# Kernel optimization log

Hardware: AMD Instinct MI355X
Metric: run time of the kernel (lower is better)

## Reference

```python
import jax, jax.numpy as jnp
import numpy as np
from jax import lax

DIM = 512
D_STATE = 16
D_CONV = 4
EXPAND = 2
E = EXPAND * DIM  # expanded_dim


def setup_inputs() -> dict:
    key = jax.random.key(0)
    ks = jax.random.split(key, 8)
    B_, L = 4, 2048
    x = jax.random.normal(ks[0], (B_, L, DIM), dtype=jnp.float32)
    # parameters (xavier-ish scaled random; exact init values don't matter for math)
    W_in = jax.random.normal(ks[1], (2 * E, DIM), dtype=jnp.float32) * (1.0 / np.sqrt(DIM))
    W_conv = jax.random.normal(ks[2], (E, 1, D_CONV), dtype=jnp.float32) * 0.3
    A = jax.random.normal(ks[3], (E, D_STATE), dtype=jnp.float32) * 0.5
    Bp = jax.random.normal(ks[4], (E, D_STATE), dtype=jnp.float32) * (1.0 / np.sqrt(D_STATE))
    Cp = jax.random.normal(ks[5], (E, D_STATE), dtype=jnp.float32) * (1.0 / np.sqrt(D_STATE))
    Dp = jnp.zeros((E,), dtype=jnp.float32)
    W_out = jax.random.normal(ks[6], (DIM, E), dtype=jnp.float32) * (1.0 / np.sqrt(E))
    return {"x": x, "W_in": W_in, "W_conv": W_conv, "A": A, "Bp": Bp, "Cp": Cp, "Dp": Dp, "W_out": W_out}


def reference(x, W_in, W_conv, A, Bp, Cp, Dp, W_out):
    residual = x
    b, l, _ = x.shape
    xp = jnp.einsum('bld,ed->ble', x, W_in)        # [b,l,2E]
    xs, gate = jnp.split(xp, 2, axis=-1)
    xs = xs * jax.nn.sigmoid(gate)                 # [b,l,E]
    # causal depthwise conv1d: torch pads both sides by K-1 then slices [:, :, :l]
    xc = lax.conv_general_dilated(
        xs.transpose(0, 2, 1), W_conv,
        window_strides=(1,), padding=[(D_CONV - 1, 0)],
        feature_group_count=E,
        dimension_numbers=('NCH', 'OIH', 'NCH'))     # [b,E,l]
    u = jax.nn.silu(xc.transpose(0, 2, 1))          # [b,l,E]
    Aneg = -jnp.exp(A)                              # [E,N]
    delta = jax.nn.sigmoid(jnp.einsum('bld,dn->bln', u, Bp))  # [b,l,N]
    A_bar = jnp.exp(jnp.einsum('dn,bln->bldn', Aneg, delta))  # [b,l,E,N]
    Bx = jnp.einsum('bln,dn->bldn', delta, Bp) * u[..., None]  # B_bar * x_t

    def step(h, inp):
        A_t, Bx_t = inp
        h = A_t * h + Bx_t                          # [b,E,N]
        y_t = jnp.einsum('bdn,dn->bd', h, Cp)
        return h, y_t

    h0 = jnp.zeros((b, E, D_STATE), dtype=x.dtype)
    _, ys = lax.scan(step, h0, (A_bar.transpose(1, 0, 2, 3), Bx.transpose(1, 0, 2, 3)))
    y = ys.transpose(1, 0, 2)                       # [b,l,E]
    y = y + Dp * u
    out = jnp.einsum('ble,de->bld', y, W_out)
    return out + residual
```

## Files before the change

### kernel.cpp

```cpp
#include <hip/hip_runtime.h>

#define DIM   512
#define EE    1024
#define NS    16
#define BB    4
#define LL    2048
#define MM    (BB*LL)
#define NC    64
#define CL    32

typedef __bf16 bf16x8 __attribute__((ext_vector_type(8)));
typedef __bf16 bf16x4 __attribute__((ext_vector_type(4)));
typedef float  f32x4  __attribute__((ext_vector_type(4)));

static __device__ __forceinline__ float sigmoidf_(float x) {
    return 1.0f / (1.0f + __expf(-x));
}

#define GLOAD(gp, lp) __builtin_amdgcn_global_load_lds( \
    (const __attribute__((address_space(1))) unsigned int*)(const void*)(gp), \
    (__attribute__((address_space(3))) unsigned int*)(void*)(lp), 16, 0, 0)

__global__ __launch_bounds__(256) void k_tobf(
    const float* __restrict__ x, const float* __restrict__ Win,
    const float* __restrict__ Wout, const float* __restrict__ Bp,
    __bf16* __restrict__ xbf, __bf16* __restrict__ winbf,
    __bf16* __restrict__ woutbf, __bf16* __restrict__ bpT)
{
    int g = blockIdx.x * 256 + threadIdx.x;
    const int nx4 = MM * DIM / 4;
    const int nw4 = 2 * EE * DIM / 4;
    const int no4 = DIM * EE / 4;
    if (g < nx4) {
        f32x4 v = ((const f32x4*)x)[g];
        bf16x4 o; for (int j = 0; j < 4; ++j) o[j] = (__bf16)v[j];
        ((bf16x4*)xbf)[g] = o;
    } else if (g < nx4 + nw4) {
        int i = g - nx4;
        f32x4 v = ((const f32x4*)Win)[i];
        bf16x4 o; for (int j = 0; j < 4; ++j) o[j] = (__bf16)v[j];
        ((bf16x4*)winbf)[i] = o;
    } else if (g < nx4 + nw4 + no4) {
        int i = g - nx4 - nw4;
        f32x4 v = ((const f32x4*)Wout)[i];
        bf16x4 o; for (int j = 0; j < 4; ++j) o[j] = (__bf16)v[j];
        ((bf16x4*)woutbf)[i] = o;
    } else {
        int i = g - nx4 - nw4 - no4;
        int e = i >> 4, n = i & 15;
        bpT[n * EE + e] = (__bf16)Bp[i];
    }
}

__global__ __launch_bounds__(256, 4) void k_gemm1(
    const __bf16* __restrict__ Abf,
    const __bf16* __restrict__ Wbf,
    __bf16* __restrict__ xs)
{
    __shared__ __bf16 sA[128 * 64];
    __shared__ __bf16 sB0[64 * 64];
    __shared__ __bf16 sB1[64 * 64];

    int bid = blockIdx.x;
    int swz = (bid & 7) * 128 + (bid >> 3);
    int bm = swz >> 4;
    int bn = swz & 15;

    int t = threadIdx.x;
    int lane = t & 63;
    int w = t >> 6;
    int wm = (w >> 1) * 64;
    int wn = (w & 1) * 32;
    int r15 = lane & 15;
    int kq = lane >> 4;

    const __bf16* Agb  = Abf + (bm * 128) * DIM;
    const __bf16* B0gb = Wbf + (bn * 64) * DIM;
    const __bf16* B1gb = Wbf + (1024 + bn * 64) * DIM;

    f32x4 accx[4][2] = {};
    f32x4 accg[4][2] = {};

    for (int kt = 0; kt < 8; ++kt) {
        #pragma unroll
        for (int i_ = 0; i_ < 4; ++i_) {
            int c_ = i_ * 256 + t;
            int row_ = c_ >> 3;
            int ss_ = (c_ & 7) ^ (row_ & 7);
            GLOAD(Agb + kt * 64 + row_ * DIM + ss_ * 8, sA + (i_ * 256 + w * 64) * 8);
        }
        #pragma unroll
        for (int i_ = 0; i_ < 2; ++i_) {
            int c_ = i_ * 256 + t;
            int row_ = c_ >> 3;
            int ss_ = (c_ & 7) ^ (row_ & 7);
            GLOAD(B0gb + kt * 64 + row_ * DIM + ss_ * 8, sB0 + (i_ * 256 + w * 64) * 8);
            GLOAD(B1gb + kt * 64 + row_ * DIM + ss_ * 8, sB1 + (i_ * 256 + w * 64) * 8);
        }
        __syncthreads();
        #pragma unroll
        for (int ks = 0; ks < 2; ++ks) {
            int kcs = ks * 4 + kq;
            bf16x8 a[4], b0[2], b1[2];
            #pragma unroll
            for (int m = 0; m < 4; ++m) {
                int r = wm + m * 16 + r15;
                a[m] = *(const bf16x8*)&sA[r * 64 + (kcs ^ (r & 7)) * 8];
            }
            #pragma unroll
            for (int n = 0; n < 2; ++n) {
                int r = wn + n * 16 + r15;
                b0[n] = *(const bf16x8*)&sB0[r * 64 + (kcs ^ (r & 7)) * 8];
                b1[n] = *(const bf16x8*)&sB1[r * 64 + (kcs ^ (r & 7)) * 8];
            }
            #pragma unroll
            for (int m = 0; m < 4; ++m)
                #pragma unroll
                for (int n = 0; n < 2; ++n) {
                    accx[m][n] = __builtin_amdgcn_mfma_f32_16x16x32_bf16(a[m], b0[n], accx[m][n], 0, 0, 0);
                    accg[m][n] = __builtin_amdgcn_mfma_f32_16x16x32_bf16(a[m], b1[n], accg[m][n], 0, 0, 0);
                }
        }
        __syncthreads();
    }

    #pragma unroll
    for (int m = 0; m < 4; ++m)
        #pragma unroll
        for (int n = 0; n < 2; ++n)
            #pragma unroll
            for (int r = 0; r < 4; ++r) {
                int row = bm * 128 + wm + m * 16 + (lane >> 4) * 4 + r;
                int col = bn * 64 + wn + n * 16 + r15;
                float xv = accx[m][n][r];
                float gv = accg[m][n][r];
                xs[row * EE + col] = (__bf16)(xv * sigmoidf_(gv));
            }
}

__global__ __launch_bounds__(256) void k_convdelta(
    const __bf16* __restrict__ xs, const float* __restrict__ Wc,
    const __bf16* __restrict__ bpT,
    __bf16* __restrict__ u, float* __restrict__ delta)
{
    __shared__ __bf16 uS[8][1032];
    __shared__ float red[4][256];
    int bid = blockIdx.x;
    int r0b = bid * 8;
    int t = threadIdx.x;
    int cg = t & 127, rh = t >> 7;
    int e8 = cg << 3;
    int rr0 = r0b + rh * 4;
    int l0 = rr0 & (LL - 1);

    f32x4 wj[8];
    #pragma unroll
    for (int j = 0; j < 8; ++j) wj[j] = *(const f32x4*)&Wc[(e8 + j) * 4];
    bf16x8 z = {};
    bf16x8 win[7];
    #pragma unroll
    for (int i = 0; i < 7; ++i) {
        win[i] = (l0 + i >= 3) ? *(const bf16x8*)&xs[(rr0 + i - 3) * EE + e8] : z;
    }
    #pragma unroll
    for (int i = 0; i < 4; ++i) {
        bf16x8 out;
        #pragma unroll
        for (int j = 0; j < 8; ++j) {
            float a = (float)win[i][j] * wj[j][0] + (float)win[i + 1][j] * wj[j][1]
                    + (float)win[i + 2][j] * wj[j][2] + (float)win[i + 3][j] * wj[j][3];
            out[j] = (__bf16)(a * sigmoidf_(a));
        }
        *(bf16x8*)&u[(rr0 + i) * EE + e8] = out;
        *(bf16x8*)&uS[rh * 4 + i][e8] = out;
    }
    __syncthreads();

    int lane = t & 63, w = t >> 6;
    int ar = lane & 15, kc = (lane >> 4) << 3;
    f32x4 acc = {};
    #pragma unroll
    for (int k0 = 0; k0 < 256; k0 += 32) {
        int k = w * 256 + k0 + kc;
        bf16x8 a = *(const bf16x8*)&uS[ar & 7][k];
        bf16x8 b = *(const bf16x8*)&bpT[ar * EE + k];
        acc = __builtin_amdgcn_mfma_f32_16x16x32_bf16(a, b, acc, 0, 0, 0);
    }
    *(f32x4*)&red[w][lane * 4] = acc;
    __syncthreads();
    if (t < 32) {
        #pragma unroll
        for (int r = 0; r < 4; ++r) {
            float s = red[0][t * 4 + r] + red[1][t * 4 + r]
                    + red[2][t * 4 + r] + red[3][t * 4 + r];
            int row = (t >> 4) * 4 + r;
            int col = t & 15;
            delta[(r0b + row) * NS + col] = sigmoidf_(s);
        }
    }
}

__global__ __launch_bounds__(64) void k_dsum(
    const float* __restrict__ delta, float* __restrict__ Dsum)
{
    int g = blockIdx.x * 64 + threadIdx.x;
    int n = g & 15, c = (g >> 4) & (NC - 1), b = g >> 10;
    int base = (b * LL + c * CL) * NS + n;
    float s = 0.f;
    #pragma unroll
    for (int l = 0; l < CL; ++l) s += delta[base + l * NS];
    Dsum[(b * NC + c) * NS + n] = s;
}

__global__ __launch_bounds__(256) void k_scan1(
    const __bf16* __restrict__ u, const float* __restrict__ delta,
    const float* __restrict__ A, const float* __restrict__ Bp,
    const float* __restrict__ Cp, const float* __restrict__ Dp,
    float* __restrict__ hbuf, __bf16* __restrict__ yloc)
{
    int bid = blockIdx.x;
    int et = bid & 3;
    int c  = (bid >> 2) & (NC - 1);
    int b  = bid >> 8;
    int t  = threadIdx.x;
    int e  = et * 256 + t;
    __shared__ float dls[CL * NS];
    int sbase = (b * LL + c * CL) * NS;
    for (int i = t; i < CL * NS; i += 256) dls[i] = delta[sbase + i];
    __syncthreads();

    float Ae[NS], Bpr[NS], Cr[NS];
    #pragma unroll
    for (int q = 0; q < 4; ++q) {
        f32x4 av = *(const f32x4*)&A[e * NS + q * 4];
        f32x4 bv = *(const f32x4*)&Bp[e * NS + q * 4];
        f32x4 cv = *(const f32x4*)&Cp[e * NS + q * 4];
        #pragma unroll
        for (int j = 0; j < 4; ++j) {
            Ae[q * 4 + j]  = -__expf(av[j]) * 1.44269504f;
            Bpr[q * 4 + j] = bv[j];
            Cr[q * 4 + j]  = cv[j];
        }
    }
    float Dv = Dp[e];
    float h[NS] = {};
    const __bf16* up = &u[(b * LL + c * CL) * EE + e];
    __bf16* yp = &yloc[(b * LL + c * CL) * EE + e];
    for (int l = 0; l < CL; ++l) {
        float uv = (float)up[l * EE];
        float yv = Dv * uv;
        const f32x4* dr = (const f32x4*)&dls[l * NS];
        f32x4 dv[4] = {dr[0], dr[1], dr[2], dr[3]};
        #pragma unroll
        for (int j = 0; j < NS; ++j) {
            float d  = dv[j >> 2][j & 3];
            float ab = __builtin_amdgcn_exp2f(Ae[j] * d);
            h[j] = ab * h[j] + (d * Bpr[j]) * uv;
            yv += h[j] * Cr[j];
        }
        yp[l * EE] = (__bf16)yv;
    }
    int base = ((b * NC + c) * EE + e) * NS;
    #pragma unroll
    for (int q = 0; q < 4; ++q) {
        f32x4 hv = {h[q * 4 + 0], h[q * 4 + 1], h[q * 4 + 2], h[q * 4 + 3]};
        *(f32x4*)&hbuf[base + q * 4] = hv;
    }
}

__global__ __launch_bounds__(256) void k_fix(
    const float* __restrict__ A, const float* __restrict__ Dsum,
    float* __restrict__ hbuf)
{
    int g = blockIdx.x * 256 + threadIdx.x;
    int b = g >> 14;
    int r = g & 16383;
    int n = r & 15;
    float Ae = -__expf(A[r]) * 1.44269504f;
    float h = 0.f;
    for (int c = 0; c < NC; ++c) {
        int idx = (b * NC + c) * (EE * NS) + r;
        float hl = hbuf[idx];
        float P  = __builtin_amdgcn_exp2f(Ae * Dsum[(b * NC + c) * NS + n]);
        hbuf[idx] = h;
        h = P * h + hl;
    }
}

__global__ __launch_bounds__(256) void k_scan2(
    const float* __restrict__ delta, const float* __restrict__ A,
    const float* __restrict__ Cp, const float* __restrict__ hin,
    __bf16* __restrict__ y)
{
    int bid = blockIdx.x;
    int et = bid & 3;
    int c  = (bid >> 2) & (NC - 1);
    int b  = bid >> 8;
    if (c == 0) return;
    int t  = threadIdx.x;
    int e  = et * 256 + t;
    __shared__ float dls[CL * NS];
    int sbase = (b * LL + c * CL) * NS;
    for (int i = t; i < CL * NS; i += 256) dls[i] = delta[sbase + i];
    __syncthreads();

    int base = ((b * NC + c) * EE + e) * NS;
    float Ae[NS], g_[NS];
    #pragma unroll
    for (int q = 0; q < 4; ++q) {
        f32x4 av = *(const f32x4*)&A[e * NS + q * 4];
        f32x4 cv = *(const f32x4*)&Cp[e * NS + q * 4];
        f32x4 hv = *(const f32x4*)&hin[base + q * 4];
        #pragma unroll
        for (int j = 0; j < 4; ++j) {
            Ae[q * 4 + j] = -__expf(av[j]) * 1.44269504f;
            g_[q * 4 + j] = cv[j] * hv[j];
        }
    }
    float D[NS] = {};
    __bf16* yp = &y[(b * LL + c * CL) * EE + e];
    for (int l = 0; l < CL; ++l) {
        const f32x4* dr = (const f32x4*)&dls[l * NS];
        f32x4 dv[4] = {dr[0], dr[1], dr[2], dr[3]};
        float corr = 0.f;
        #pragma unroll
        for (int j = 0; j < NS; ++j) {
            D[j] += dv[j >> 2][j & 3];
            corr += g_[j] * __builtin_amdgcn_exp2f(Ae[j] * D[j]);
        }
        float yv = (float)yp[l * EE] + corr;
        yp[l * EE] = (__bf16)yv;
    }
}

__global__ __launch_bounds__(256, 2) void k_gemm2(
    const __bf16* __restrict__ Ybf,
    const __bf16* __restrict__ Wobf,
    const float* __restrict__ xres,
    float* __restrict__ out)
{
    __shared__ __bf16 sA[128 * 64];
    __shared__ __bf16 sB[64 * 64];

    int bid = blockIdx.x;
    int swz = (bid & 7) * 64 + (bid >> 3);
    int bm = swz >> 3;
    int bn = swz & 7;

    int t = threadIdx.x;
    int lane = t & 63;
    int w = t >> 6;
    int wm = (w >> 1) * 64;
    int wn = (w & 1) * 32;
    int r15 = lane & 15;
    int kq = lane >> 4;

    const __bf16* Agb = Ybf + (bm * 128) * EE;
    const __bf16* Bgb = Wobf + (bn * 64) * EE;

    f32x4 acc[4][2] = {};

    for (int kt = 0; kt < 16; ++kt) {
        #pragma unroll
        for (int i_ = 0; i_ < 4; ++i_) {
            int c_ = i_ * 256 + t;
            int row_ = c_ >> 3;
            int ss_ = (c_ & 7) ^ (row_ & 7);
            GLOAD(Agb + kt * 64 + row_ * EE + ss_ * 8, sA + (i_ * 256 + w * 64) * 8);
        }
        #pragma unroll
        for (int i_ = 0; i_ < 2; ++i_) {
            int c_ = i_ * 256 + t;
            int row_ = c_ >> 3;
            int ss_ = (c_ & 7) ^ (row_ & 7);
            GLOAD(Bgb + kt * 64 + row_ * EE + ss_ * 8, sB + (i_ * 256 + w * 64) * 8);
        }
        __syncthreads();
        #pragma unroll
        for (int ks = 0; ks < 2; ++ks) {
            int kcs = ks * 4 + kq;
            bf16x8 a[4], b[2];
            #pragma unroll
            for (int m = 0; m < 4; ++m) {
                int r = wm + m * 16 + r15;
                a[m] = *(const bf16x8*)&sA[r * 64 + (kcs ^ (r & 7)) * 8];
            }
            #pragma unroll
            for (int n = 0; n < 2; ++n) {
                int r = wn + n * 16 + r15;
                b[n] = *(const bf16x8*)&sB[r * 64 + (kcs ^ (r & 7)) * 8];
            }
            #pragma unroll
            for (int m = 0; m < 4; ++m)
                #pragma unroll
                for (int n = 0; n < 2; ++n)
                    acc[m][n] = __builtin_amdgcn_mfma_f32_16x16x32_bf16(a[m], b[n], acc[m][n], 0, 0, 0);
        }
        __syncthreads();
    }

    #pragma unroll
    for (int m = 0; m < 4; ++m)
        #pragma unroll
        for (int n = 0; n < 2; ++n)
            #pragma unroll
            for (int r = 0; r < 4; ++r) {
                int row = bm * 128 + wm + m * 16 + (lane >> 4) * 4 + r;
                int col = bn * 64 + wn + n * 16 + r15;
                out[row * DIM + col] = acc[m][n][r] + xres[row * DIM + col];
            }
}

extern "C" void kernel_launch(void* const* d_in, const int* in_sizes, int n_in,
                              void* d_out, int out_size, void* d_ws, size_t ws_size,
                              hipStream_t stream) {
    const float* x    = (const float*)d_in[0];
    const float* Win  = (const float*)d_in[1];
    const float* Wc   = (const float*)d_in[2];
    const float* A    = (const float*)d_in[3];
    const float* Bp   = (const float*)d_in[4];
    const float* Cp   = (const float*)d_in[5];
    const float* Dp   = (const float*)d_in[6];
    const float* Wout = (const float*)d_in[7];

    char* ws = (char*)d_ws;
    __bf16* woutbf = (__bf16*)(ws + 0);
    __bf16* bpT    = (__bf16*)(ws + 1048576);
    float*  delta  = (float*)(ws + 1081344);
    float*  Dsum   = (float*)(ws + 1605632);
    __bf16* ubf    = (__bf16*)(ws + 1622016);
    __bf16* xbf    = (__bf16*)(ws + 18399232);
    __bf16* winbf  = (__bf16*)(ws + 26787840);
    __bf16* xsbf   = (__bf16*)(ws + 28884992);
    __bf16* yloc   = (__bf16*)(ws + 28884992);
    float*  hbuf   = (float*)(ws + 45662208);

    k_tobf     <<<5696, 256, 0, stream>>>(x, Win, Wout, Bp, xbf, winbf, woutbf, bpT);
    k_gemm1    <<<1024, 256, 0, stream>>>(xbf, winbf, xsbf);
    k_convdelta<<<1024, 256, 0, stream>>>(xsbf, Wc, bpT, ubf, delta);
    k_dsum     <<<64, 64, 0, stream>>>(delta, Dsum);
    k_scan1    <<<1024, 256, 0, stream>>>(ubf, delta, A, Bp, Cp, Dp, hbuf, yloc);
    k_fix      <<<256, 256, 0, stream>>>(A, Dsum, hbuf);
    k_scan2    <<<1024, 256, 0, stream>>>(delta, A, Cp, hbuf, yloc);
    k_gemm2    <<<512, 256, 0, stream>>>(yloc, woutbf, x, (float*)d_out);
}
```

Measured before the change: 142.8 us.

## Fold chunk delta-sum into scan1, halve chunk count, store carry states in fp16

The chunked scan now uses 32 chunks of 64 steps instead of 64 of 32, which halves the carry-state traffic and the serial fix-up length but gives scan kernels half as many blocks. The separate delta-sum kernel is removed and that sum is computed inside scan1 from shared memory. Inter-chunk state buffers are stored as fp16 instead of fp32, and the output GEMM reads the residual from the bf16 copy of x instead of fp32. Together these cut global memory traffic and one launch, at the cost of fp16 and bf16 rounding in the carried state and the residual.

Measured after the change: 149.9 us. 1.05x slower.

```diff
diff --git a/kernel.cpp b/kernel.cpp
--- a/kernel.cpp
+++ b/kernel.cpp
@@ -6,12 +6,13 @@
 #define BB    4
 #define LL    2048
 #define MM    (BB*LL)
-#define NC    64
-#define CL    32
+#define NC    32
+#define CL    64
 
 typedef __bf16 bf16x8 __attribute__((ext_vector_type(8)));
 typedef __bf16 bf16x4 __attribute__((ext_vector_type(4)));
 typedef float  f32x4  __attribute__((ext_vector_type(4)));
+typedef _Float16 f16x8 __attribute__((ext_vector_type(8)));
 
 static __device__ __forceinline__ float sigmoidf_(float x) {
     return 1.0f / (1.0f + __expf(-x));
@@ -148,8 +149,8 @@
     int bid = blockIdx.x;
     int r0b = bid * 8;
     int t = threadIdx.x;
-    int cg = t & 127, rh = t >> 7;
-    int e8 = cg << 3;
+    int cg_ = t & 127, rh = t >> 7;
+    int e8 = cg_ << 3;
     int rr0 = r0b + rh * 4;
     int l0 = rr0 & (LL - 1);
 
@@ -200,34 +201,30 @@
     }
 }
 
-__global__ __launch_bounds__(64) void k_dsum(
-    const float* __restrict__ delta, float* __restrict__ Dsum)
-{
-    int g = blockIdx.x * 64 + threadIdx.x;
-    int n = g & 15, c = (g >> 4) & (NC - 1), b = g >> 10;
-    int base = (b * LL + c * CL) * NS + n;
-    float s = 0.f;
-    #pragma unroll
-    for (int l = 0; l < CL; ++l) s += delta[base + l * NS];
-    Dsum[(b * NC + c) * NS + n] = s;
-}
-
 __global__ __launch_bounds__(256) void k_scan1(
     const __bf16* __restrict__ u, const float* __restrict__ delta,
     const float* __restrict__ A, const float* __restrict__ Bp,
     const float* __restrict__ Cp, const float* __restrict__ Dp,
-    float* __restrict__ hbuf, __bf16* __restrict__ yloc)
+    _Float16* __restrict__ hbuf, float* __restrict__ Dsum,
+    __bf16* __restrict__ yloc)
 {
     int bid = blockIdx.x;
     int et = bid & 3;
     int c  = (bid >> 2) & (NC - 1);
-    int b  = bid >> 8;
+    int b  = bid >> 7;
     int t  = threadIdx.x;
     int e  = et * 256 + t;
     __shared__ float dls[CL * NS];
     int sbase = (b * LL + c * CL) * NS;
     for (int i = t; i < CL * NS; i += 256) dls[i] = delta[sbase + i];
     __syncthreads();
+
+    if (et == 0 && t < NS) {
+        float s = 0.f;
+        #pragma unroll
+        for (int l = 0; l < CL; ++l) s += dls[l * NS + t];
+        Dsum[(b * NC + c) * NS + t] = s;
+    }
 
     float Ae[NS], Bpr[NS], Cr[NS];
     #pragma unroll
@@ -261,16 +258,16 @@
         yp[l * EE] = (__bf16)yv;
     }
     int base = ((b * NC + c) * EE + e) * NS;
-    #pragma unroll
-    for (int q = 0; q < 4; ++q) {
-        f32x4 hv = {h[q * 4 + 0], h[q * 4 + 1], h[q * 4 + 2], h[q * 4 + 3]};
-        *(f32x4*)&hbuf[base + q * 4] = hv;
-    }
+    f16x8 h0, h1;
+    #pragma unroll
+    for (int j = 0; j < 8; ++j) { h0[j] = (_Float16)h[j]; h1[j] = (_Float16)h[8 + j]; }
+    *(f16x8*)&hbuf[base] = h0;
+    *(f16x8*)&hbuf[base + 8] = h1;
 }
 
 __global__ __launch_bounds__(256) void k_fix(
     const float* __restrict__ A, const float* __restrict__ Dsum,
-    float* __restrict__ hbuf)
+    _Float16* __restrict__ hbuf)
 {
     int g = blockIdx.x * 256 + threadIdx.x;
     int b = g >> 14;
@@ -280,22 +277,22 @@
     float h = 0.f;
     for (int c = 0; c < NC; ++c) {
         int idx = (b * NC + c) * (EE * NS) + r;
-        float hl = hbuf[idx];
+        float hl = (float)hbuf[idx];
         float P  = __builtin_amdgcn_exp2f(Ae * Dsum[(b * NC + c) * NS + n]);
-        hbuf[idx] = h;
+        hbuf[idx] = (_Float16)h;
         h = P * h + hl;
     }
 }
 
 __global__ __launch_bounds__(256) void k_scan2(
     const float* __restrict__ delta, const float* __restrict__ A,
-    const float* __restrict__ Cp, const float* __restrict__ hin,
+    const float* __restrict__ Cp, const _Float16* __restrict__ hin,
     __bf16* __restrict__ y)
 {
     int bid = blockIdx.x;
     int et = bid & 3;
     int c  = (bid >> 2) & (NC - 1);
-    int b  = bid >> 8;
+    int b  = bid >> 7;
     if (c == 0) return;
     int t  = threadIdx.x;
     int e  = et * 256 + t;
@@ -305,16 +302,19 @@
     __syncthreads();
 
     int base = ((b * NC + c) * EE + e) * NS;
+    f16x8 hv0 = *(const f16x8*)&hin[base];
+    f16x8 hv1 = *(const f16x8*)&hin[base + 8];
     float Ae[NS], g_[NS];
     #pragma unroll
     for (int q = 0; q < 4; ++q) {
         f32x4 av = *(const f32x4*)&A[e * NS + q * 4];
         f32x4 cv = *(const f32x4*)&Cp[e * NS + q * 4];
-        f32x4 hv = *(const f32x4*)&hin[base + q * 4];
         #pragma unroll
         for (int j = 0; j < 4; ++j) {
-            Ae[q * 4 + j] = -__expf(av[j]) * 1.44269504f;
-            g_[q * 4 + j] = cv[j] * hv[j];
+            int jj = q * 4 + j;
+            Ae[jj] = -__expf(av[j]) * 1.44269504f;
+            float hvv = (jj < 8) ? (float)hv0[jj & 7] : (float)hv1[jj & 7];
+            g_[jj] = cv[j] * hvv;
         }
     }
     float D[NS] = {};
@@ -336,7 +336,7 @@
 __global__ __launch_bounds__(256, 2) void k_gemm2(
     const __bf16* __restrict__ Ybf,
     const __bf16* __restrict__ Wobf,
-    const float* __restrict__ xres,
+    const __bf16* __restrict__ xres,
     float* __restrict__ out)
 {
     __shared__ __bf16 sA[128 * 64];
@@ -379,7 +379,7 @@
         #pragma unroll
         for (int ks = 0; ks < 2; ++ks) {
             int kcs = ks * 4 + kq;
-            bf16x8 a[4], b[2];
+            bf16x8 a[4], bfr[2];
             #pragma unroll
             for (int m = 0; m < 4; ++m) {
                 int r = wm + m * 16 + r15;
@@ -388,13 +388,13 @@
             #pragma unroll
             for (int n = 0; n < 2; ++n) {
                 int r = wn + n * 16 + r15;
-                b[n] = *(const bf16x8*)&sB[r * 64 + (kcs ^ (r & 7)) * 8];
+                bfr[n] = *(const bf16x8*)&sB[r * 64 + (kcs ^ (r & 7)) * 8];
             }
             #pragma unroll
             for (int m = 0; m < 4; ++m)
                 #pragma unroll
                 for (int n = 0; n < 2; ++n)
-                    acc[m][n] = __builtin_amdgcn_mfma_f32_16x16x32_bf16(a[m], b[n], acc[m][n], 0, 0, 0);
+                    acc[m][n] = __builtin_amdgcn_mfma_f32_16x16x32_bf16(a[m], bfr[n], acc[m][n], 0, 0, 0);
         }
         __syncthreads();
     }
@@ -407,7 +407,7 @@
             for (int r = 0; r < 4; ++r) {
                 int row = bm * 128 + wm + m * 16 + (lane >> 4) * 4 + r;
                 int col = bn * 64 + wn + n * 16 + r15;
-                out[row * DIM + col] = acc[m][n][r] + xres[row * DIM + col];
+                out[row * DIM + col] = acc[m][n][r] + (float)xres[row * DIM + col];
             }
 }
 
@@ -433,14 +433,13 @@
     __bf16* winbf  = (__bf16*)(ws + 26787840);
     __bf16* xsbf   = (__bf16*)(ws + 28884992);
     __bf16* yloc   = (__bf16*)(ws + 28884992);
-    float*  hbuf   = (float*)(ws + 45662208);
+    _Float16* hbuf = (_Float16*)(ws + 45662208);
 
     k_tobf     <<<5696, 256, 0, stream>>>(x, Win, Wout, Bp, xbf, winbf, woutbf, bpT);
     k_gemm1    <<<1024, 256, 0, stream>>>(xbf, winbf, xsbf);
     k_convdelta<<<1024, 256, 0, stream>>>(xsbf, Wc, bpT, ubf, delta);
-    k_dsum     <<<64, 64, 0, stream>>>(delta, Dsum);
-    k_scan1    <<<1024, 256, 0, stream>>>(ubf, delta, A, Bp, Cp, Dp, hbuf, yloc);
+    k_scan1    <<<512, 256, 0, stream>>>(ubf, delta, A, Bp, Cp, Dp, hbuf, Dsum, yloc);
     k_fix      <<<256, 256, 0, stream>>>(A, Dsum, hbuf);
-    k_scan2    <<<1024, 256, 0, stream>>>(delta, A, Cp, hbuf, yloc);
-    k_gemm2    <<<512, 256, 0, stream>>>(yloc, woutbf, x, (float*)d_out);
-}
+    k_scan2    <<<512, 256, 0, stream>>>(delta, A, Cp, hbuf, yloc);
+    k_gemm2    <<<512, 256, 0, stream>>>(yloc, woutbf, xbf, (float*)d_out);
+}
```
